# Kernel optimization log

Measured on AMD Instinct MI355X. Metric: run time of the kernel, lower is better.

The kernel has to match this reference:

```python
import jax, jax.numpy as jnp
import numpy as np

N = 30000; E = 480000; B = 60
IN = 200; ID = 128; H = 128
NEXP = 4; TOPK = 2; TEMP = 1.5
HEADS = 4; DH = H // HEADS


def _ln(x, g, b):
    mu = jnp.mean(x, -1, keepdims=True)
    var = jnp.var(x, -1, keepdims=True)
    return (x - mu) / jnp.sqrt(var + 1e-5) * g + b


def _seg_sum(d, i, n):
    return jax.ops.segment_sum(d, i, num_segments=n)


def setup_inputs():
    key = jax.random.key(0)
    kit = iter(jax.random.split(key, 80))
    def w(*s):
        return jax.random.normal(next(kit), s, jnp.float32) * 0.05
    inp = {}
    inp['x'] = jax.random.normal(next(kit), (N, IN), jnp.float32)
    inp['node_identity'] = jax.random.normal(next(kit), (N, ID), jnp.float32)
    inp['edge_index'] = jax.random.randint(next(kit), (2, E), 0, N)
    inp['batch'] = jnp.sort(jax.random.randint(next(kit), (N,), 0, B))
    inp.update(fe_W=w(IN, H), fe_b=jnp.zeros(H), fe_g=jnp.ones(H), fe_be=jnp.zeros(H))
    inp.update(ie_W=w(ID, H), ie_b=jnp.zeros(H), ie_g=jnp.ones(H), ie_be=jnp.zeros(H))
    inp.update(fuse_W=w(2 * H, H), fuse_b=jnp.zeros(H), fuse_g=jnp.ones(H), fuse_be=jnp.zeros(H))
    inp.update(router_W=w(2 * H, NEXP))
    inp.update(mlp_W1=w(H, H), mlp_b1=jnp.zeros(H), mlp_W2=w(H, H), mlp_b2=jnp.zeros(H))
    inp.update(cheb_W=w(2, 2, H, H), cheb_b=jnp.zeros((2, H)))
    inp.update(gt_Wq=w(2, H, H), gt_bq=jnp.zeros((2, H)), gt_Wk=w(2, H, H), gt_bk=jnp.zeros((2, H)),
               gt_Wv=w(2, H, H), gt_bv=jnp.zeros((2, H)), gt_Ws=w(2, H, H), gt_bs=jnp.zeros((2, H)))
    inp.update(gcn_W=w(2, H, H), gcn_b=jnp.zeros((2, H)))
    inp.update(pn_g=jnp.ones((NEXP, H)), pn_b=jnp.zeros((NEXP, H)), expert_scales=jnp.ones(NEXP))
    inp.update(h1_W=w(H, H), h1_b=jnp.zeros(H), h1_g=jnp.ones(H), h1_be=jnp.zeros(H))
    inp.update(h2_W=w(H, H // 2), h2_b=jnp.zeros(H // 2), h2_g=jnp.ones(H // 2), h2_be=jnp.zeros(H // 2))
    inp.update(h3_W=w(H // 2, 2), h3_b=jnp.zeros(2), logit_bias=jnp.zeros(2))
    return inp


def _forward(x, node_identity, edge_index, batch, fe_W, fe_b, fe_g, fe_be, ie_W, ie_b, ie_g, ie_be,
             fuse_W, fuse_b, fuse_g, fuse_be, router_W, mlp_W1, mlp_b1, mlp_W2, mlp_b2, cheb_W, cheb_b,
             gt_Wq, gt_bq, gt_Wk, gt_bk, gt_Wv, gt_bv, gt_Ws, gt_bs, gcn_W, gcn_b, pn_g, pn_b,
             expert_scales, h1_W, h1_b, h1_g, h1_be, h2_W, h2_b, h2_g, h2_be, h3_W, h3_b, logit_bias):
    relu = jax.nn.relu
    src, dst = edge_index[0], edge_index[1]
    # encoders + fuse
    h_x = relu(_ln(x @ fe_W + fe_b, fe_g, fe_be))
    h_id = relu(_ln(node_identity @ ie_W + ie_b, ie_g, ie_be))
    h_router = jnp.concatenate([h_x, h_id], -1)
    h = relu(_ln(h_router @ fuse_W + fuse_b, fuse_g, fuse_be))
    # noisy top-k router (eval: no noise, no dropout)
    node_logits = h_router @ router_W
    probs = jax.nn.softmax(node_logits / TEMP, -1)
    vals, idx = jax.lax.top_k(probs, TOPK)
    wts = vals / jnp.clip(jnp.sum(vals, -1, keepdims=True), 1e-9)
    gates = jnp.zeros_like(probs).at[jnp.arange(N)[:, None], idx].set(wts)  # [N, 4]
    # degree / normalization terms
    ones_e = jnp.ones(E, jnp.float32)
    deg = _seg_sum(ones_e, dst, N)
    dinv = jnp.where(deg > 0, jax.lax.rsqrt(jnp.maximum(deg, 1.0)), 0.0)
    dinvl = jax.lax.rsqrt(deg + 1.0)  # with self loops (GCN)
    enorm = dinv[src] * dinv[dst]
    enorml = dinvl[src] * dinvl[dst]
    def aprop(xx, en, di_self=None):
        out = _seg_sum(xx[src] * en[:, None], dst, N)
        if di_self is not None:
            out = out + xx * di_self[:, None]
        return out
    # Expert 0: MLP (2 layers)
    e0 = relu(h @ mlp_W1 + mlp_b1) @ mlp_W2 + mlp_b2
    # Expert 1: ChebNet K=2 (lambda_max=2 -> L_hat = -A_norm), 2 layers
    z = h
    for l in range(2):
        tx1 = -aprop(z, enorm)
        z = z @ cheb_W[l, 0] + tx1 @ cheb_W[l, 1] + cheb_b[l]
        if l == 0:
            z = relu(z)
    e1 = z
    # Expert 2: Graph Transformer, 2 layers, heads=4, root-weight skip
    z = h
    for l in range(2):
        q = (z @ gt_Wq[l] + gt_bq[l]).reshape(N, HEADS, DH)
        k = (z @ gt_Wk[l] + gt_bk[l]).reshape(N, HEADS, DH)
        v = (z @ gt_Wv[l] + gt_bv[l]).reshape(N, HEADS, DH)
        logits = jnp.sum(q[dst] * k[src], -1) * (1.0 / DH ** 0.5)  # [E, heads]
        m = jax.ops.segment_max(logits, dst, num_segments=N)
        m = jnp.where(jnp.isfinite(m), m, 0.0)
        p = jnp.exp(logits - m[dst])
        denom = jnp.clip(_seg_sum(p, dst, N), 1e-9)
        attn = p / denom[dst]
        agg = _seg_sum(attn[:, :, None] * v[src], dst, N).reshape(N, H)
        z = agg + z @ gt_Ws[l] + gt_bs[l]
        if l == 0:
            z = relu(z)
    e2 = z
    # Expert 3: GCN, 2 layers, self loops
    z = h
    for l in range(2):
        zw = z @ gcn_W[l]
        z = aprop(zw, enorml, dinvl * dinvl) + gcn_b[l]
        if l == 0:
            z = relu(z)
    e3 = z
    # per-expert post-norm, scale, gated combine + residual
    eo = jnp.stack([e0, e1, e2, e3], 0)  # [4, N, H]
    eo = _ln(eo, pn_g[:, None, :], pn_b[:, None, :]) * expert_scales[:, None, None]
    out = h + jnp.einsum('ne,enh->nh', gates, eo)
    # mean-pool readout per graph
    counts = jnp.clip(_seg_sum(jnp.ones(N, jnp.float32), batch, B), 1.0)
    pooled = _seg_sum(out, batch, B) / counts[:, None]
    # classification head
    zc = relu(_ln(pooled @ h1_W + h1_b, h1_g, h1_be))
    zc = relu(_ln(zc @ h2_W + h2_b, h2_g, h2_be))
    return zc @ h3_W + h3_b + logit_bias


def reference(x, node_identity, edge_index, batch, fe_W, fe_b, fe_g, fe_be, ie_W, ie_b, ie_g, ie_be,
              fuse_W, fuse_b, fuse_g, fuse_be, router_W, mlp_W1, mlp_b1, mlp_W2, mlp_b2, cheb_W, cheb_b,
              gt_Wq, gt_bq, gt_Wk, gt_bk, gt_Wv, gt_bv, gt_Ws, gt_bs, gcn_W, gcn_b, pn_g, pn_b,
              expert_scales, h1_W, h1_b, h1_g, h1_be, h2_W, h2_b, h2_g, h2_be, h3_W, h3_b, logit_bias):
    return _forward(x, node_identity, edge_index, batch, fe_W, fe_b, fe_g, fe_be, ie_W, ie_b, ie_g, ie_be,
                    fuse_W, fuse_b, fuse_g, fuse_be, router_W, mlp_W1, mlp_b1, mlp_W2, mlp_b2, cheb_W, cheb_b,
                    gt_Wq, gt_bq, gt_Wk, gt_bk, gt_Wv, gt_bv, gt_Ws, gt_bs, gcn_W, gcn_b, pn_g, pn_b,
                    expert_scales, h1_W, h1_b, h1_g, h1_be, h2_W, h2_b, h2_g, h2_be, h3_W, h3_b, logit_bias)
```

## Files before the change

### kernel.cpp

```cpp
#include <hip/hip_runtime.h>

#define PCH   32
#define NWT   19
#define SCH   2048

typedef unsigned short ushort_t;
typedef __attribute__((ext_vector_type(8))) short bf16x8;
typedef __attribute__((ext_vector_type(4))) float f32x4;

__device__ __forceinline__ float bf2f(unsigned int v) {
    return __uint_as_float(v << 16);
}
__device__ __forceinline__ unsigned int f2bu(float f) {
    unsigned int u = __float_as_uint(f);
    return (u + 0x7fffu + ((u >> 16) & 1u)) >> 16;
}
__device__ __forceinline__ void unpack8(uint4 u, float* f) {
    f[0] = bf2f(u.x & 0xffff); f[1] = bf2f(u.x >> 16);
    f[2] = bf2f(u.y & 0xffff); f[3] = bf2f(u.y >> 16);
    f[4] = bf2f(u.z & 0xffff); f[5] = bf2f(u.z >> 16);
    f[6] = bf2f(u.w & 0xffff); f[7] = bf2f(u.w >> 16);
}
__device__ __forceinline__ uint4 pack8(const float* f) {
    uint4 p;
// ... 552 lines not shown
        const ushort_t* Wrow = (ph ? Wt2 : Wt1) + (size_t)sbn * K;
        for (int k0 = 0; k0 < K; k0 += 32) {
            uint4 apk = arow_ok ? *(const uint4*)(Arow + k0 + sak) : make_uint4(0, 0, 0, 0);
            uint4 b0 = *(const uint4*)(Wrow + k0 + sbk);
            uint4 b1 = *(const uint4*)(Wrow + k0 + sbk + 8);
            __syncthreads();
            *(uint4*)&As[sar][sak] = apk;
            *(uint4*)&Bs[sbn][sbk] = b0;
            *(uint4*)&Bs[sbn][sbk + 8] = b1;
            __syncthreads();
            bf16x8 af = *(const bf16x8*)&As[16 * wv + l16][q * 8];
#pragma unroll
            for (int t = 0; t < 8; t++) {
                bf16x8 bf = *(const bf16x8*)&Bs[t * 16 + l16][q * 8];
                acc[t] = __builtin_amdgcn_mfma_f32_16x16x32_bf16(af, bf, acc[t], 0, 0, 0);
            }
        }
    }
#pragma unroll
    for (int t = 0; t < 8; t++) {
        int col = t * 16 + l16;
        float bb = bias ? bias[col] : 0.f;
#pragma unroll
        for (int r = 0; r < 4; r++) {
            int row = m0 + 16 * wv + q * 4 + r;
            float val = acc[t][r] + bb;
            if (relu) val = fmaxf(val, 0.f);
            float other = __shfl_xor(val, 1);
            if (!(lane & 1) && row < M) {
                unsigned int pk = f2bu(val) | (f2bu(other) << 16);
                *(unsigned int*)(Cb + (size_t)row * 128 + col) = pk;
            }
        }
    }
}

__device__ __forceinline__ void gemm_wv_dev(const ushort_t* __restrict__ A,
                                            const ushort_t* __restrict__ Wt,
                                            ushort_t* __restrict__ Cb, int M,
                                            const float* __restrict__ bias, int relu,
                                            int w, int lane)
{
    const int K = 128;
    int ct = w & 3;
    int rt = w >> 2;
    int row0 = rt * 16;
    if (row0 >= M) return;
    int l16 = lane & 15, q = lane >> 4;
    int arow = row0 + l16;
    bool aok = arow < M;
    const ushort_t* Ar = A + (size_t)arow * K + q * 8;
    const ushort_t* W0 = Wt + (size_t)(ct * 32 + l16) * K + q * 8;
    const ushort_t* W1 = W0 + (size_t)16 * K;
    bf16x8 zz = {0, 0, 0, 0, 0, 0, 0, 0};
    f32x4 a0 = {0.f, 0.f, 0.f, 0.f}, a1 = {0.f, 0.f, 0.f, 0.f};
#pragma unroll
    for (int k0 = 0; k0 < K; k0 += 32) {
        bf16x8 af = aok ? *(const bf16x8*)(Ar + k0) : zz;
        bf16x8 b0 = *(const bf16x8*)(W0 + k0);
        bf16x8 b1 = *(const bf16x8*)(W1 + k0);
        a0 = __builtin_amdgcn_mfma_f32_16x16x32_bf16(af, b0, a0, 0, 0, 0);
        a1 = __builtin_amdgcn_mfma_f32_16x16x32_bf16(af, b1, a1, 0, 0, 0);
    }
    f32x4 av[2] = {a0, a1};
#pragma unroll
    for (int t = 0; t < 2; t++) {
        int col = ct * 32 + t * 16 + l16;
        float bb = bias ? bias[col] : 0.f;
#pragma unroll
        for (int r = 0; r < 4; r++) {
            int row = row0 + q * 4 + r;
            float val = av[t][r] + bb;
            if (relu) val = fmaxf(val, 0.f);
            float other = __shfl_xor(val, 1);
            if (!(l16 & 1) && row < M) {
                unsigned int pk = f2bu(val) | (f2bu(other) << 16);
                *(unsigned int*)(Cb + (size_t)row * 128 + col) = pk;
            }
        }
    }
}

__device__ __forceinline__ void gather2_dev(const ushort_t* __restrict__ Xb,
                                            ushort_t* __restrict__ OutA, ushort_t* __restrict__ OutB,
                                            const int* __restrict__ rowptr, const int* __restrict__ csr,
                                            const float* __restrict__ ecA, const float* __restrict__ ecB,
                                            const float* __restrict__ dinvl, int M, int bx)
{
    int node = bx * 4 + (threadIdx.x >> 6);
    int lane = threadIdx.x & 63;
    if (node >= M) return;
    int beg = rowptr[node], end = rowptr[node + 1];
    int slot = lane >> 4, g = lane & 15;
    float aA[8] = {0, 0, 0, 0, 0, 0, 0, 0};
    float aB[8] = {0, 0, 0, 0, 0, 0, 0, 0};

    float cAa = 0.f, cBa = 0.f, cAb = 0.f, cBb = 0.f;
    int na = 0, nb = 0;
    float nAa = 0.f, nBa = 0.f, nAb = 0.f, nBb = 0.f;
    uint4 xA, xB;
    {
        int r0 = beg + slot, r1 = beg + 4 + slot;
        int ia = 0, ib = 0;
        if (r0 < end) { ia = csr[r0]; cAa = ecA[r0]; cBa = ecB[r0]; }
        if (r1 < end) { ib = csr[r1]; cAb = ecA[r1]; cBb = ecB[r1]; }
        xA = *(const uint4*)(Xb + (size_t)ia * 128 + g * 8);
        xB = *(const uint4*)(Xb + (size_t)ib * 128 + g * 8);
    }
    {
        int r0 = beg + 8 + slot, r1 = beg + 12 + slot;
        if (r0 < end) { na = csr[r0]; nAa = ecA[r0]; nBa = ecB[r0]; }
        if (r1 < end) { nb = csr[r1]; nAb = ecA[r1]; nBb = ecB[r1]; }
    }
    for (int e = beg; e < end; e += 8) {
        uint4 xA2 = *(const uint4*)(Xb + (size_t)na * 128 + g * 8);
        uint4 xB2 = *(const uint4*)(Xb + (size_t)nb * 128 + g * 8);
        int r0 = e + 16 + slot, r1 = e + 20 + slot;
        int ma = 0, mb = 0;
        float mAa = 0.f, mBa = 0.f, mAb = 0.f, mBb = 0.f;
        if (r0 < end) { ma = csr[r0]; mAa = ecA[r0]; mBa = ecB[r0]; }
        if (r1 < end) { mb = csr[r1]; mAb = ecA[r1]; mBb = ecB[r1]; }
        fma8(xA, cAa, aA); fma8(xA, cBa, aB);
        fma8(xB, cAb, aA); fma8(xB, cBb, aB);
        xA = xA2; xB = xB2;
        cAa = nAa; cBa = nBa; cAb = nAb; cBb = nBb;
        na = ma; nb = mb;
        nAa = mAa; nBa = mBa; nAb = mAb; nBb = mBb;
    }
#pragma unroll
    for (int j = 0; j < 8; j++) {
        aA[j] += __shfl_xor(aA[j], 16); aA[j] += __shfl_xor(aA[j], 32);
        aB[j] += __shfl_xor(aB[j], 16); aB[j] += __shfl_xor(aB[j], 32);
    }
    {
        float c = dinvl[node]; c *= c;
        uint4 xs = *(const uint4*)(Xb + (size_t)node * 128 + g * 8);
        fma8(xs, c, aB);
    }
    if (lane < 16) {
        float oA[8], oB[8];
#pragma unroll
        for (int j = 0; j < 8; j++) { oA[j] = -aA[j]; oB[j] = aB[j]; }
        size_t ofs = (size_t)node * 128 + g * 8;
        *(uint4*)(OutA + ofs) = pack8(oA);
        *(uint4*)(OutB + ofs) = pack8(oB);
    }
}

__device__ __forceinline__ void gather_l2_dev(const ushort_t* __restrict__ XA,
                                              const ushort_t* __restrict__ XB,
                                              ushort_t* __restrict__ OutA, ushort_t* __restrict__ OutB,
                                              const int* __restrict__ rowptr, const int* __restrict__ csr,
                                              const float* __restrict__ ecA, const float* __restrict__ ecB,
                                              const float* __restrict__ dinvl, int M, int bx)
{
    int node = bx * 4 + (threadIdx.x >> 6);
    int lane = threadIdx.x & 63;
    if (node >= M) return;
    int beg = rowptr[node], end = rowptr[node + 1];
    int slot = lane >> 4, g = lane & 15;
    float aA[8] = {0, 0, 0, 0, 0, 0, 0, 0};
    float aB[8] = {0, 0, 0, 0, 0, 0, 0, 0};

    float cAa = 0.f, cBa = 0.f, cAb = 0.f, cBb = 0.f;
    int na = 0, nb = 0;
    float nAa = 0.f, nBa = 0.f, nAb = 0.f, nBb = 0.f;
    uint4 ra, rb, sa, sb;
    {
        int r0 = beg + slot, r1 = beg + 4 + slot;
        int ia = 0, ib = 0;
        if (r0 < end) { ia = csr[r0]; cAa = ecA[r0]; cBa = ecB[r0]; }
        if (r1 < end) { ib = csr[r1]; cAb = ecA[r1]; cBb = ecB[r1]; }
        ra = *(const uint4*)(XA + (size_t)ia * 128 + g * 8);
        rb = *(const uint4*)(XA + (size_t)ib * 128 + g * 8);
        sa = *(const uint4*)(XB + (size_t)ia * 128 + g * 8);
        sb = *(const uint4*)(XB + (size_t)ib * 128 + g * 8);
    }
    {
        int r0 = beg + 8 + slot, r1 = beg + 12 + slot;
        if (r0 < end) { na = csr[r0]; nAa = ecA[r0]; nBa = ecB[r0]; }
        if (r1 < end) { nb = csr[r1]; nAb = ecA[r1]; nBb = ecB[r1]; }
    }
    for (int e = beg; e < end; e += 8) {
        uint4 ra2 = *(const uint4*)(XA + (size_t)na * 128 + g * 8);
        uint4 rb2 = *(const uint4*)(XA + (size_t)nb * 128 + g * 8);
        uint4 sa2 = *(const uint4*)(XB + (size_t)na * 128 + g * 8);
        uint4 sb2 = *(const uint4*)(XB + (size_t)nb * 128 + g * 8);
        int r0 = e + 16 + slot, r1 = e + 20 + slot;
        int ma = 0, mb = 0;
        float mAa = 0.f, mBa = 0.f, mAb = 0.f, mBb = 0.f;
        if (r0 < end) { ma = csr[r0]; mAa = ecA[r0]; mBa = ecB[r0]; }
        if (r1 < end) { mb = csr[r1]; mAb = ecA[r1]; mBb = ecB[r1]; }
        fma8(ra, cAa, aA); fma8(rb, cAb, aA);
        fma8(sa, cBa, aB); fma8(sb, cBb, aB);
        ra = ra2; rb = rb2; sa = sa2; sb = sb2;
        cAa = nAa; cBa = nBa; cAb = nAb; cBb = nBb;
        na = ma; nb = mb;
        nAa = mAa; nBa = mBa; nAb = mAb; nBb = mBb;
    }
#pragma unroll
    for (int j = 0; j < 8; j++) {
        aA[j] += __shfl_xor(aA[j], 16); aA[j] += __shfl_xor(aA[j], 32);
        aB[j] += __shfl_xor(aB[j], 16); aB[j] += __shfl_xor(aB[j], 32);
    }
    {
        float c = dinvl[node]; c *= c;
        uint4 xs = *(const uint4*)(XB + (size_t)node * 128 + g * 8);
        fma8(xs, c, aB);
    }
    if (lane < 16) {
        float oA[8], oB[8];
#pragma unroll
        for (int j = 0; j < 8; j++) { oA[j] = -aA[j]; oB[j] = aB[j]; }
        size_t ofs = (size_t)node * 128 + g * 8;
        *(uint4*)(OutA + ofs) = pack8(oA);
        *(uint4*)(OutB + ofs) = pack8(oB);
    }
}

__device__ __forceinline__ void gt_attn_dev(const ushort_t* __restrict__ Qb,
                                            const ushort_t* __restrict__ KV,
                                            const int* __restrict__ rowptr, const int* __restrict__ csr,
                                            const ushort_t* __restrict__ sk, int relu,
                                            ushort_t* __restrict__ Outb, int M, int bx)
{
    const float SCL = 0.17677669529663689f * 1.4426950408889634f;
    int node = bx * 4 + (threadIdx.x >> 6);
    int lane = threadIdx.x & 63;
    if (node >= M) return;
    int beg = rowptr[node], end = rowptr[node + 1];
    int slot = lane >> 4, g = lane & 15;
    uint4 qv = *(const uint4*)(Qb + (size_t)node * 128 + g * 8);
    float qf[8];
    unpack8(qv, qf);
#pragma unroll
    for (int j = 0; j < 8; j++) qf[j] *= SCL;
    float ax[8] = {0, 0, 0, 0, 0, 0, 0, 0};
    float den = 0.f;

    bool va = false, vb = false;
    int na = 0, nb = 0;
    bool wa = false, wb = false;
    uint4 kA, kB, uA, uB;
    {
        int r0 = beg + slot, r1 = beg + 4 + slot;
        va = r0 < end; vb = r1 < end;
        int ia = va ? csr[r0] : 0;
        int ib = vb ? csr[r1] : 0;
        const ushort_t* p0 = KV + (size_t)ia * 256 + g * 8;
        const ushort_t* p1 = KV + (size_t)ib * 256 + g * 8;
        kA = *(const uint4*)p0; uA = *(const uint4*)(p0 + 128);
        kB = *(const uint4*)p1; uB = *(const uint4*)(p1 + 128);
    }
    {
        int r0 = beg + 8 + slot, r1 = beg + 12 + slot;
        wa = r0 < end; wb = r1 < end;
        na = wa ? csr[r0] : 0;
        nb = wb ? csr[r1] : 0;
    }
    for (int e = beg; e < end; e += 8) {
        const ushort_t* p0 = KV + (size_t)na * 256 + g * 8;
        const ushort_t* p1 = KV + (size_t)nb * 256 + g * 8;
        uint4 kA2 = *(const uint4*)p0;
        uint4 uA2 = *(const uint4*)(p0 + 128);
        uint4 kB2 = *(const uint4*)p1;
        uint4 uB2 = *(const uint4*)(p1 + 128);
        int r0 = e + 16 + slot, r1 = e + 20 + slot;
        bool xa = r0 < end, xb = r1 < end;
        int ma = xa ? csr[r0] : 0;
        int mb = xb ? csr[r1] : 0;
        float d0 = dot8(kA, qf);
        float d1 = dot8(kB, qf);
        d0 += __shfl_xor(d0, 1); d0 += __shfl_xor(d0, 2);
        d1 += __shfl_xor(d1, 1); d1 += __shfl_xor(d1, 2);
        float w0 = va ? exp2f(fminf(d0, 80.f)) : 0.f;
        float w1 = vb ? exp2f(fminf(d1, 80.f)) : 0.f;
        den += w0 + w1;
        fma8(uA, w0, ax);
        fma8(uB, w1, ax);
        kA = kA2; kB = kB2; uA = uA2; uB = uB2;
        va = wa; vb = wb;
        wa = xa; wb = xb; na = ma; nb = mb;
    }
#pragma unroll
    for (int j = 0; j < 8; j++) {
        ax[j] += __shfl_xor(ax[j], 16); ax[j] += __shfl_xor(ax[j], 32);
    }
    den += __shfl_xor(den, 16); den += __shfl_xor(den, 32);
    float dd = fmaxf(den, 1e-9f);
    if (lane < 16) {
        uint4 sv = *(const uint4*)(sk + (size_t)node * 128 + g * 8);
        float sf[8];
        unpack8(sv, sf);
        float o[8];
#pragma unroll
        for (int j = 0; j < 8; j++) {
            float v = ax[j] / dd + sf[j];
            o[j] = relu ? fmaxf(v, 0.f) : v;
        }
        *(uint4*)(Outb + (size_t)node * 128 + g * 8) = pack8(o);
    }
}

__global__ __launch_bounds__(256)
void flatA_kernel(const ushort_t* __restrict__ hb,
                  ushort_t* __restrict__ x1, ushort_t* __restrict__ x2,
                  const int* __restrict__ rowptr, const int* __restrict__ csr,
                  const float* __restrict__ ecA, const float* __restrict__ ecB,
                  const float* __restrict__ dinvl, int N,
                  const ushort_t* __restrict__ wmlp1, ushort_t* __restrict__ xm,
                  const float* __restrict__ b18,
                  const ushort_t* __restrict__ wqkvs,
                  ushort_t* __restrict__ qb, ushort_t* __restrict__ kvb,
                  ushort_t* __restrict__ skb,
                  const float* __restrict__ bq, const float* __restrict__ bk,
                  const float* __restrict__ bv, const float* __restrict__ bs)
{
    __shared__ ushort_t As[64][40];
    __shared__ ushort_t Bs[128][40];
    int bx = blockIdx.x;
    int gN4 = (N + 3) >> 2;
    int RT = (N + 15) >> 4;
    int gG = (N + 63) >> 6;
    const size_t PS = (size_t)128 * 128;
    if (bx < gN4) {
        gather2_dev(hb, x1, x2, rowptr, csr, ecA, ecB, dinvl, N, bx);
    } else if (bx < gN4 + RT) {
        int w = (bx - gN4) * 4 + (threadIdx.x >> 6);
        gemm_wv_dev(hb, wmlp1, xm, N, b18, 1, w, threadIdx.x & 63);
    } else {
        int b2 = bx - gN4 - RT;
        int pan = b2 / gG;
        int gx = b2 - pan * gG;
        if (pan == 0) gemm_bfs_dev(As, Bs, hb, wqkvs, qb, 128, N, bq, gx);
        else if (pan == 1) gemm_bfs_dev(As, Bs, hb, wqkvs + PS, kvb, 256, N, bk, gx);
        else if (pan == 2) gemm_bfs_dev(As, Bs, hb, wqkvs + 2 * PS, kvb + 128, 256, N, bv, gx);
        else gemm_bfs_dev(As, Bs, hb, wqkvs + 3 * PS, skb, 128, N, bs, gx);
    }
}

__global__ __launch_bounds__(256)
void megaA_kernel(const ushort_t* __restrict__ hb,
                  const ushort_t* __restrict__ wch0,
                  const ushort_t* __restrict__ x1, const ushort_t* __restrict__ wch1,
                  ushort_t* __restrict__ x0, const float* __restrict__ bch,
                  const ushort_t* __restrict__ x2, const ushort_t* __restrict__ wgcn,
                  ushort_t* __restrict__ xg1, const float* __restrict__ bgcn,
                  int M)
{
    __shared__ ushort_t As[64][40];
    __shared__ ushort_t Bs[128][40];
    if (blockIdx.y == 0)
        gemm_dual_dev(As, Bs, hb, wch0, x1, wch1, x0, M, bch, 1, blockIdx.x);
    else
        gemm_bf_dev<128>(As, Bs, x2, wgcn, xg1, M, bgcn, 1, blockIdx.x);
}

__global__ void flatB_kernel(const ushort_t* __restrict__ qb, const ushort_t* __restrict__ kvb,
                             const int* __restrict__ rowptr, const int* __restrict__ csr,
                             const ushort_t* __restrict__ skb, ushort_t* __restrict__ aout,
                             const ushort_t* __restrict__ x0, const ushort_t* __restrict__ xg1,
                             ushort_t* __restrict__ x3, ushort_t* __restrict__ x2,
                             const float* __restrict__ ecA, const float* __restrict__ ecB,
                             const float* __restrict__ dinvl, int N,
                             const ushort_t* __restrict__ xm, const ushort_t* __restrict__ wmlp2,
                             ushort_t* __restrict__ e0b, const float* __restrict__ bmlp2)
{
    int bx = blockIdx.x;
    int gN4 = (N + 3) >> 2;
    if (bx < gN4) gt_attn_dev(qb, kvb, rowptr, csr, skb, 1, aout, N, bx);
    else if (bx < 2 * gN4) gather_l2_dev(x0, xg1, x3, x2, rowptr, csr, ecA, ecB, dinvl, N, bx - gN4);
    else {
        int w = (bx - 2 * gN4) * 4 + (threadIdx.x >> 6);
        gemm_wv_dev(xm, wmlp2, e0b, N, bmlp2, 0, w, threadIdx.x & 63);
    }
}

__global__ __launch_bounds__(256)
void megaB_kernel(const ushort_t* __restrict__ x1,
                  const ushort_t* __restrict__ wqkvs,
                  ushort_t* __restrict__ qb, ushort_t* __restrict__ kvb, ushort_t* __restrict__ skb,
                  const float* __restrict__ bq, const float* __restrict__ bk,
                  const float* __restrict__ bv, const float* __restrict__ bs,
                  const ushort_t* __restrict__ x0, const ushort_t* __restrict__ wch0,
                  const ushort_t* __restrict__ x3, const ushort_t* __restrict__ wch1,
                  ushort_t* __restrict__ e1b, const float* __restrict__ bch,
                  const ushort_t* __restrict__ x2, const ushort_t* __restrict__ wgcn,
                  ushort_t* __restrict__ e3b, const float* __restrict__ bgcn,
                  int M)
{
    __shared__ ushort_t As[64][40];
    __shared__ ushort_t Bs[128][40];
    int y = blockIdx.y, bx = blockIdx.x;
    const size_t PS = (size_t)128 * 128;
    if (y == 0) gemm_bfs_dev(As, Bs, x1, wqkvs, qb, 128, M, bq, bx);
    else if (y == 1) gemm_bfs_dev(As, Bs, x1, wqkvs + PS, kvb, 256, M, bk, bx);
    else if (y == 2) gemm_bfs_dev(As, Bs, x1, wqkvs + 2 * PS, kvb + 128, 256, M, bv, bx);
    else if (y == 3) gemm_bfs_dev(As, Bs, x1, wqkvs + 3 * PS, skb, 128, M, bs, bx);
    else if (y == 4) gemm_dual_dev(As, Bs, x0, wch0, x3, wch1, e1b, M, bch, 0, bx);
    else gemm_bf_dev<128>(As, Bs, x2, wgcn, e3b, M, bgcn, 0, bx);
}

__global__ void attn2_pool_kernel(const ushort_t* __restrict__ Qb, const ushort_t* __restrict__ KV,
                                  const int* __restrict__ rowptr, const int* __restrict__ csr,
                                  const ushort_t* __restrict__ sk, ushort_t* __restrict__ e2b,
                                  int N,
                                  const ushort_t* __restrict__ hb,
                                  const ushort_t* __restrict__ e0, const ushort_t* __restrict__ e1,
                                  const ushort_t* __restrict__ e3,
                                  const float* __restrict__ gates,
                                  const float* __restrict__ png, const float* __restrict__ pnb,
                                  const float* __restrict__ esc,
                                  const int* __restrict__ bstart, const int* __restrict__ bend,
                                  float* __restrict__ partial)
{
    int bx = blockIdx.x;
    int gN4 = (N + 3) >> 2;
    if (bx < gN4) {
        gt_attn_dev(Qb, KV, rowptr, csr, sk, 0, e2b, N, bx);
        return;
    }
    int idx = bx - gN4;
    int b = idx >> 3;
    int cq = ((idx & 7) << 2) + (threadIdx.x >> 6);
    int lane = threadIdx.x & 63;
    int s0 = bstart[b], eN = bend[b];
    const ushort_t* eps[3] = {e0, e1, e3};
    const int eid[3] = {0, 1, 3};
    float ga[3], gb[3], ba[3], bb[3], es[3];
#pragma unroll
    for (int j = 0; j < 3; j++) {
        int ee = eid[j];
        ga[j] = png[ee * 128 + lane * 2];
        gb[j] = png[ee * 128 + lane * 2 + 1];
        ba[j] = pnb[ee * 128 + lane * 2];
        bb[j] = pnb[ee * 128 + lane * 2 + 1];
        es[j] = esc[ee];
    }
    float sx = 0.f, sy = 0.f;
    for (int n = s0 + cq; n < eN; n += PCH) {
        size_t ofs = (size_t)n * 128 + lane * 2;
        float4 gg = *(const float4*)(gates + (size_t)n * 4);
        float gv[3] = {gg.x, gg.y, gg.w};
        unsigned int hu = *(const unsigned int*)(hb + ofs);
        float ox = bf2f(hu & 0xffff), oy = bf2f(hu >> 16);
#pragma unroll
        for (int j = 0; j < 3; j++) {
            unsigned int u = *(const unsigned int*)(eps[j] + ofs);
            float vx = bf2f(u & 0xffff), vy = bf2f(u >> 16);
            float su = vx + vy, sq = vx * vx + vy * vy;
#pragma unroll
            for (int off = 32; off; off >>= 1) { su += __shfl_xor(su, off); sq += __shfl_xor(sq, off); }
            float mean = su * (1.f / 128.f);
            float var = sq * (1.f / 128.f) - mean * mean;
            float inv = rsqrtf(var + 1e-5f);
            float cc = es[j] * gv[j];
            ox = fmaf(cc, (vx - mean) * inv * ga[j] + ba[j], ox);
            oy = fmaf(cc, (vy - mean) * inv * gb[j] + bb[j], oy);
        }
        sx += ox; sy += oy;
    }
    *(float2*)(partial + ((size_t)b * PCH + cq) * 128 + lane * 2) = make_float2(sx, sy);
}

__global__ void poolB_kernel(const ushort_t* __restrict__ e2,
                             const float* __restrict__ gates,
                             const float* __restrict__ png, const float* __restrict__ pnb,
                             const float* __restrict__ esc,
                             const int* __restrict__ bstart, const int* __restrict__ bend,
                             float* __restrict__ partial2)
{
    int idx = blockIdx.x;
    int b = idx >> 3;
    int cq = ((idx & 7) << 2) + (threadIdx.x >> 6);
    int lane = threadIdx.x & 63;
    int s0 = bstart[b], eN = bend[b];
    float ga = png[2 * 128 + lane * 2], gb = png[2 * 128 + lane * 2 + 1];
    float ba = pnb[2 * 128 + lane * 2], bb = pnb[2 * 128 + lane * 2 + 1];
    float es = esc[2];
    float sx = 0.f, sy = 0.f;
    for (int n = s0 + cq; n < eN; n += PCH) {
        size_t ofs = (size_t)n * 128 + lane * 2;
        float gv = gates[(size_t)n * 4 + 2];
        unsigned int u = *(const unsigned int*)(e2 + ofs);
        float vx = bf2f(u & 0xffff), vy = bf2f(u >> 16);
        float su = vx + vy, sq = vx * vx + vy * vy;
#pragma unroll
        for (int off = 32; off; off >>= 1) { su += __shfl_xor(su, off); sq += __shfl_xor(sq, off); }
        float mean = su * (1.f / 128.f);
        float var = sq * (1.f / 128.f) - mean * mean;
        float inv = rsqrtf(var + 1e-5f);
        float cc = es * gv;
        sx = fmaf(cc, (vx - mean) * inv * ga + ba, sx);
        sy = fmaf(cc, (vy - mean) * inv * gb + bb, sy);
    }
    *(float2*)(partial2 + ((size_t)b * PCH + cq) * 128 + lane * 2) = make_float2(sx, sy);
}

__global__ void head_kernel(const float* __restrict__ partial,
                            const float* __restrict__ partial2,
                            const int* __restrict__ bstart, const int* __restrict__ bend,
                            const float* __restrict__ h1W, const float* __restrict__ h1b,
                            const float* __restrict__ h1g, const float* __restrict__ h1be,
                            const float* __restrict__ h2W, const float* __restrict__ h2b,
                            const float* __restrict__ h2g, const float* __restrict__ h2be,
                            const float* __restrict__ h3W, const float* __restrict__ h3b,
                            const float* __restrict__ lbias,
                            float* __restrict__ out, int B)
{
    __shared__ float p[128], z[128];
    int b = blockIdx.x, t = threadIdx.x;
    float sum = 0.f;
#pragma unroll
    for (int c = 0; c < PCH; c++) {
        size_t o = ((size_t)b * PCH + c) * 128 + t;
        sum += partial[o] + partial2[o];
    }
    float cnt = fmaxf((float)(bend[b] - bstart[b]), 1.f);
    p[t] = sum / cnt;
    __syncthreads();
    float a = h1b[t];
    for (int k = 0; k < 128; k++) a = fmaf(p[k], h1W[k * 128 + t], a);
    z[t] = a;
    __syncthreads();
    float s = 0.f, sq = 0.f;
    for (int k = 0; k < 128; k++) { float x = z[k]; s += x; sq += x * x; }
    float mean = s * (1.f / 128.f), var = sq * (1.f / 128.f) - mean * mean;
    float y = fmaxf((a - mean) * rsqrtf(var + 1e-5f) * h1g[t] + h1be[t], 0.f);
    __syncthreads();
    z[t] = y;
    __syncthreads();
    float a2 = 0.f;
    if (t < 64) {
        a2 = h2b[t];
        for (int k = 0; k < 128; k++) a2 = fmaf(z[k], h2W[k * 64 + t], a2);
    }
    __syncthreads();
    if (t < 64) p[t] = a2;
    __syncthreads();
    if (t < 2) {
        float s2 = 0.f, sq2 = 0.f;
        for (int k = 0; k < 64; k++) { float x = p[k]; s2 += x; sq2 += x * x; }
        float mean2 = s2 * (1.f / 64.f), var2 = sq2 * (1.f / 64.f) - mean2 * mean2;
        float inv2 = rsqrtf(var2 + 1e-5f);
        float o = h3b[t] + lbias[t];
        for (int k = 0; k < 64; k++) {
            float zc = fmaxf((p[k] - mean2) * inv2 * h2g[k] + h2be[k], 0.f);
            o = fmaf(zc, h3W[k * 2 + t], o);
        }
        out[b * 2 + t] = o;
    }
}

extern "C" void kernel_launch(void* const* d_in, const int* in_sizes, int n_in,
                              void* d_out, int out_size, void* d_ws, size_t ws_size,
                              hipStream_t stream)
{
    (void)ws_size; (void)n_in;
    const int N = in_sizes[3];
    const int E = in_sizes[2] / 2;
    const int B = out_size / 2;

    const int* ei = (const int*)d_in[2];
    const int* src = ei;
    const int* dst = ei + E;
    const int* batch = (const int*)d_in[3];

    const float* W[47];
    for (int i = 0; i < 47; i++) W[i] = (const float*)d_in[i];

    size_t fN = (size_t)N;
    float* gates    = (float*)d_ws;
    float* dinv     = gates + 4 * fN;
    float* dinvl    = dinv + fN;
    float* partial  = dinvl + fN;
    float* partial2 = partial + (size_t)128 * B * PCH;
    float* logitsA  = partial2 + (size_t)128 * B * PCH;
    float* logitsB  = logitsA + 4 * fN;
    ushort_t* hb  = (ushort_t*)(logitsB + 4 * fN);
    ushort_t* e0b = hb + 128 * fN;
    ushort_t* e1b = e0b + 128 * fN;
    ushort_t* e2b = e1b + 128 * fN;
    ushort_t* e3b = e2b + 128 * fN;
    ushort_t* x0  = e3b + 128 * fN;
    ushort_t* x1  = x0 + 128 * fN;
    ushort_t* x2  = x1 + 128 * fN;
    ushort_t* x3  = x2 + 128 * fN;
    ushort_t* xm  = x3 + 128 * fN;
    ushort_t* xg1 = xm + 128 * fN;
    ushort_t* skb = xg1 + 128 * fN;
    ushort_t* qb  = skb + 128 * fN;
    ushort_t* kvb = qb + 128 * fN;
    ushort_t* hrb = kvb + 256 * fN;
    ushort_t* wt  = hrb + 256 * fN;
    WtPack wp;
    const float* wsrc[NWT] = {
        W[4], W[8], W[12], W[17], W[19],
        W[21], W[21] + 16384, W[21] + 32768, W[21] + 49152,
        W[23], W[25], W[27], W[29],
        W[23] + 16384, W[25] + 16384, W[27] + 16384, W[29] + 16384,
        W[31], W[31] + 16384
    };
    const int wk[NWT] = {200, 128, 256, 128, 128,
                         128, 128, 128, 128,
                         128, 128, 128, 128,
                         128, 128, 128, 128,
                         128, 128};
    unsigned long long woff[NWT];
    unsigned long long acc_off = 0;
    for (int i = 0; i < NWT; i++) {
        wp.src[i] = wsrc[i];
        wp.K[i] = wk[i];
        wp.off[i] = acc_off;
        woff[i] = acc_off;
        acc_off += (unsigned long long)128 * wk[i];
    }
    int* degi   = (int*)(wt + acc_off + 8);
    int* cursor = degi + N;
    int* rowptr = cursor + N;
    int* csr    = rowptr + (N + 1);
    int* bstart = csr + E;
    int* bend   = bstart + B;
    int* bsum   = bend + B;
    float* ecA  = (float*)(bsum + 256);
    float* ecB  = ecA + E;

    dim3 blk(256);
    int gN4 = (N + 3) / 4;
    int gG = (N + 63) / 64;
    int RT = (N + 15) / 16;
    int nsb = (N + SCH - 1) / SCH;
    int nseg = (N + 255) / 256;
    int nedge = (E + 255) / 256;
    int npool = B * (PCH / 4);

    hipMemsetAsync(degi, 0, (size_t)2 * N * sizeof(int), stream);
    hipMemsetAsync(bstart, 0, (size_t)2 * B * sizeof(int), stream);

    setup_mega_kernel<<<dim3(608 + nseg + nedge), blk, 0, stream>>>(
        wp, wt, batch, bstart, bend, N, dst, degi, E);
    scan1_kernel<<<dim3(nsb), blk, 0, stream>>>(degi, rowptr, bsum, N);
    scan2_kernel<<<1, blk, 0, stream>>>(bsum, nsb);
    EncCfg c0 = {W[0], 200, 200, wt + woff[0], hrb, W[5], W[6], W[7], W[16], logitsA};
    EncCfg c1 = {W[1], 128, 128, wt + woff[1], hrb + 128, W[9], W[10], W[11], W[16] + 512, logitsB};
    scan3_enc_kernel<<<dim3(nseg + 2 * gG), blk, 0, stream>>>(
        rowptr, bsum, degi, dinv, dinvl, N, c0, c1);
    ln_csr_topk_kernel<<<dim3(gG + nedge + nseg), blk, 0, stream>>>(
        hrb, wt + woff[2], hb, N, W[13], W[14], W[15],
        src, dst, rowptr, cursor, csr, dinv, dinvl, ecA, ecB, E,
        logitsA, logitsB, gates);
    flatA_kernel<<<dim3(gN4 + RT + 4 * gG), blk, 0, stream>>>(
        hb, x1, x2, rowptr, csr, ecA, ecB, dinvl, N,
        wt + woff[3], xm, W[18],
        wt + woff[9], qb, kvb, skb, W[24], W[26], W[28], W[30]);
    megaA_kernel<<<dim3(gG, 2), blk, 0, stream>>>(
        hb, wt + woff[5], x1, wt + woff[6], x0, W[22],
        x2, wt + woff[17], xg1, W[32], N);
    flatB_kernel<<<dim3(2 * gN4 + RT), blk, 0, stream>>>(
        qb, kvb, rowptr, csr, skb, x1,
        x0, xg1, x3, x2, ecA, ecB, dinvl, N,
        xm, wt + woff[4], e0b, W[20]);
    megaB_kernel<<<dim3(gG, 6), blk, 0, stream>>>(
        x1, wt + woff[13], qb, kvb, skb,
        W[24] + 128, W[26] + 128, W[28] + 128, W[30] + 128,
        x0, wt + woff[7], x3, wt + woff[8], e1b, W[22] + 128,
        x2, wt + woff[18], e3b, W[32] + 128, N);
    attn2_pool_kernel<<<dim3(gN4 + npool), blk, 0, stream>>>(
        qb, kvb, rowptr, csr, skb, e2b, N,
        hb, e0b, e1b, e3b, gates, W[33], W[34], W[35], bstart, bend, partial);
    poolB_kernel<<<dim3(npool), blk, 0, stream>>>(
        e2b, gates, W[33], W[34], W[35], bstart, bend, partial2);
    head_kernel<<<dim3(B), dim3(128), 0, stream>>>(partial, partial2, bstart, bend,
        W[36], W[37], W[38], W[39],
        W[40], W[41], W[42], W[43],
        W[44], W[45], W[46],
        (float*)d_out, B);
}
```

Measured before the change: 517.5 us.

## Rebalance kernel work: move QKVS GEMMs to megaA and MLP2 into megaB

Moves the layer-1 QKVS projection GEMMs out of the mixed gather/GEMV flatA kernel into the megaA tiled-GEMM kernel. Also moves the second MLP layer from a per-row GEMV in flatB to a tiled MFMA GEMM in megaB. flatA and flatB become gather/attention-only plus the small GEMV, and the dense GEMMs are grouped in homogeneous launches that share LDS usage and launch bounds. The aim is less divergence between heterogeneous block types and a more efficient GEMM path for MLP2. The cost is that megaA grows and must wait for flatA to finish.

Result: faster. 498.1 us (-3.7%).

```diff
diff --git a/kernel.cpp b/kernel.cpp
--- a/kernel.cpp
+++ b/kernel.cpp
@@ -878,58 +878,47 @@
     }
 }
 
-__global__ __launch_bounds__(256)
-void flatA_kernel(const ushort_t* __restrict__ hb,
-                  ushort_t* __restrict__ x1, ushort_t* __restrict__ x2,
-                  const int* __restrict__ rowptr, const int* __restrict__ csr,
-                  const float* __restrict__ ecA, const float* __restrict__ ecB,
-                  const float* __restrict__ dinvl, int N,
-                  const ushort_t* __restrict__ wmlp1, ushort_t* __restrict__ xm,
-                  const float* __restrict__ b18,
-                  const ushort_t* __restrict__ wqkvs,
-                  ushort_t* __restrict__ qb, ushort_t* __restrict__ kvb,
-                  ushort_t* __restrict__ skb,
-                  const float* __restrict__ bq, const float* __restrict__ bk,
-                  const float* __restrict__ bv, const float* __restrict__ bs)
-{
-    __shared__ ushort_t As[64][40];
-    __shared__ ushort_t Bs[128][40];
+__global__ void flatA_kernel(const ushort_t* __restrict__ hb,
+                             ushort_t* __restrict__ x1, ushort_t* __restrict__ x2,
+                             const int* __restrict__ rowptr, const int* __restrict__ csr,
+                             const float* __restrict__ ecA, const float* __restrict__ ecB,
+                             const float* __restrict__ dinvl, int N,
+                             const ushort_t* __restrict__ wmlp1, ushort_t* __restrict__ xm,
+                             const float* __restrict__ b18)
+{
     int bx = blockIdx.x;
     int gN4 = (N + 3) >> 2;
-    int RT = (N + 15) >> 4;
-    int gG = (N + 63) >> 6;
-    const size_t PS = (size_t)128 * 128;
     if (bx < gN4) {
         gather2_dev(hb, x1, x2, rowptr, csr, ecA, ecB, dinvl, N, bx);
-    } else if (bx < gN4 + RT) {
+    } else {
         int w = (bx - gN4) * 4 + (threadIdx.x >> 6);
         gemm_wv_dev(hb, wmlp1, xm, N, b18, 1, w, threadIdx.x & 63);
-    } else {
-        int b2 = bx - gN4 - RT;
-        int pan = b2 / gG;
-        int gx = b2 - pan * gG;
-        if (pan == 0) gemm_bfs_dev(As, Bs, hb, wqkvs, qb, 128, N, bq, gx);
-        else if (pan == 1) gemm_bfs_dev(As, Bs, hb, wqkvs + PS, kvb, 256, N, bk, gx);
-        else if (pan == 2) gemm_bfs_dev(As, Bs, hb, wqkvs + 2 * PS, kvb + 128, 256, N, bv, gx);
-        else gemm_bfs_dev(As, Bs, hb, wqkvs + 3 * PS, skb, 128, N, bs, gx);
     }
 }
 
 __global__ __launch_bounds__(256)
 void megaA_kernel(const ushort_t* __restrict__ hb,
-                  const ushort_t* __restrict__ wch0,
-                  const ushort_t* __restrict__ x1, const ushort_t* __restrict__ wch1,
-                  ushort_t* __restrict__ x0, const float* __restrict__ bch,
+                  const ushort_t* __restrict__ wqkvs,
+                  ushort_t* __restrict__ qb, ushort_t* __restrict__ kvb, ushort_t* __restrict__ skb,
+                  const float* __restrict__ bq, const float* __restrict__ bk,
+                  const float* __restrict__ bv, const float* __restrict__ bs,
+                  const ushort_t* __restrict__ x1, const ushort_t* __restrict__ wch0,
+                  const ushort_t* __restrict__ wch1, ushort_t* __restrict__ x0,
+                  const float* __restrict__ bch,
                   const ushort_t* __restrict__ x2, const ushort_t* __restrict__ wgcn,
                   ushort_t* __restrict__ xg1, const float* __restrict__ bgcn,
                   int M)
 {
     __shared__ ushort_t As[64][40];
     __shared__ ushort_t Bs[128][40];
-    if (blockIdx.y == 0)
-        gemm_dual_dev(As, Bs, hb, wch0, x1, wch1, x0, M, bch, 1, blockIdx.x);
-    else
-        gemm_bf_dev<128>(As, Bs, x2, wgcn, xg1, M, bgcn, 1, blockIdx.x);
+    int y = blockIdx.y, bx = blockIdx.x;
+    const size_t PS = (size_t)128 * 128;
+    if (y == 0) gemm_bfs_dev(As, Bs, hb, wqkvs, qb, 128, M, bq, bx);
+    else if (y == 1) gemm_bfs_dev(As, Bs, hb, wqkvs + PS, kvb, 256, M, bk, bx);
+    else if (y == 2) gemm_bfs_dev(As, Bs, hb, wqkvs + 2 * PS, kvb + 128, 256, M, bv, bx);
+    else if (y == 3) gemm_bfs_dev(As, Bs, hb, wqkvs + 3 * PS, skb, 128, M, bs, bx);
+    else if (y == 4) gemm_dual_dev(As, Bs, hb, wch0, x1, wch1, x0, M, bch, 1, bx);
+    else gemm_bf_dev<128>(As, Bs, x2, wgcn, xg1, M, bgcn, 1, bx);
 }
 
 __global__ void flatB_kernel(const ushort_t* __restrict__ qb, const ushort_t* __restrict__ kvb,
@@ -938,18 +927,12 @@
                              const ushort_t* __restrict__ x0, const ushort_t* __restrict__ xg1,
                              ushort_t* __restrict__ x3, ushort_t* __restrict__ x2,
                              const float* __restrict__ ecA, const float* __restrict__ ecB,
-                             const float* __restrict__ dinvl, int N,
-                             const ushort_t* __restrict__ xm, const ushort_t* __restrict__ wmlp2,
-                             ushort_t* __restrict__ e0b, const float* __restrict__ bmlp2)
+                             const float* __restrict__ dinvl, int N)
 {
     int bx = blockIdx.x;
     int gN4 = (N + 3) >> 2;
     if (bx < gN4) gt_attn_dev(qb, kvb, rowptr, csr, skb, 1, aout, N, bx);
-    else if (bx < 2 * gN4) gather_l2_dev(x0, xg1, x3, x2, rowptr, csr, ecA, ecB, dinvl, N, bx - gN4);
-    else {
-        int w = (bx - 2 * gN4) * 4 + (threadIdx.x >> 6);
-        gemm_wv_dev(xm, wmlp2, e0b, N, bmlp2, 0, w, threadIdx.x & 63);
-    }
+    else gather_l2_dev(x0, xg1, x3, x2, rowptr, csr, ecA, ecB, dinvl, N, bx - gN4);
 }
 
 __global__ __launch_bounds__(256)
@@ -963,6 +946,8 @@
                   ushort_t* __restrict__ e1b, const float* __restrict__ bch,
                   const ushort_t* __restrict__ x2, const ushort_t* __restrict__ wgcn,
                   ushort_t* __restrict__ e3b, const float* __restrict__ bgcn,
+                  const ushort_t* __restrict__ xm, const ushort_t* __restrict__ wmlp2,
+                  ushort_t* __restrict__ e0b, const float* __restrict__ bmlp2,
                   int M)
 {
     __shared__ ushort_t As[64][40];
@@ -974,7 +959,8 @@
     else if (y == 2) gemm_bfs_dev(As, Bs, x1, wqkvs + 2 * PS, kvb + 128, 256, M, bv, bx);
     else if (y == 3) gemm_bfs_dev(As, Bs, x1, wqkvs + 3 * PS, skb, 128, M, bs, bx);
     else if (y == 4) gemm_dual_dev(As, Bs, x0, wch0, x3, wch1, e1b, M, bch, 0, bx);
-    else gemm_bf_dev<128>(As, Bs, x2, wgcn, e3b, M, bgcn, 0, bx);
+    else if (y == 5) gemm_bf_dev<128>(As, Bs, x2, wgcn, e3b, M, bgcn, 0, bx);
+    else gemm_bf_dev<128>(As, Bs, xm, wmlp2, e0b, M, bmlp2, 0, bx);
 }
 
 __global__ void attn2_pool_kernel(const ushort_t* __restrict__ Qb, const ushort_t* __restrict__ KV,
@@ -1225,22 +1211,21 @@
         hrb, wt + woff[2], hb, N, W[13], W[14], W[15],
         src, dst, rowptr, cursor, csr, dinv, dinvl, ecA, ecB, E,
         logitsA, logitsB, gates);
-    flatA_kernel<<<dim3(gN4 + RT + 4 * gG), blk, 0, stream>>>(
-        hb, x1, x2, rowptr, csr, ecA, ecB, dinvl, N,
-        wt + woff[3], xm, W[18],
-        wt + woff[9], qb, kvb, skb, W[24], W[26], W[28], W[30]);
-    megaA_kernel<<<dim3(gG, 2), blk, 0, stream>>>(
-        hb, wt + woff[5], x1, wt + woff[6], x0, W[22],
+    flatA_kernel<<<dim3(gN4 + RT), blk, 0, stream>>>(hb, x1, x2, rowptr, csr, ecA, ecB,
+                                                     dinvl, N, wt + woff[3], xm, W[18]);
+    megaA_kernel<<<dim3(gG, 6), blk, 0, stream>>>(
+        hb, wt + woff[9], qb, kvb, skb, W[24], W[26], W[28], W[30],
+        x1, wt + woff[5], wt + woff[6], x0, W[22],
         x2, wt + woff[17], xg1, W[32], N);
-    flatB_kernel<<<dim3(2 * gN4 + RT), blk, 0, stream>>>(
+    flatB_kernel<<<dim3(2 * gN4), blk, 0, stream>>>(
         qb, kvb, rowptr, csr, skb, x1,
-        x0, xg1, x3, x2, ecA, ecB, dinvl, N,
-        xm, wt + woff[4], e0b, W[20]);
-    megaB_kernel<<<dim3(gG, 6), blk, 0, stream>>>(
+        x0, xg1, x3, x2, ecA, ecB, dinvl, N);
+    megaB_kernel<<<dim3(gG, 7), blk, 0, stream>>>(
         x1, wt + woff[13], qb, kvb, skb,
         W[24] + 128, W[26] + 128, W[28] + 128, W[30] + 128,
         x0, wt + woff[7], x3, wt + woff[8], e1b, W[22] + 128,
-        x2, wt + woff[18], e3b, W[32] + 128, N);
+        x2, wt + woff[18], e3b, W[32] + 128,
+        xm, wt + woff[4], e0b, W[20], N);
     attn2_pool_kernel<<<dim3(gN4 + npool), blk, 0, stream>>>(
         qb, kvb, rowptr, csr, skb, e2b, N,
         hb, e0b, e1b, e3b, gates, W[33], W[34], W[35], bstart, bend, partial);
```
